# Kernel optimization log

Measured on AMD Instinct MI355X. Metric: run time of the kernel, lower is better.

The kernel has to match this reference:

```python
import jax, jax.numpy as jnp
import numpy as np
from jax import lax

B, CIN, S = 16, 1, 64          # batch, input channels, spatial
C = 16                          # c_out hidden channels
T = 50                          # ODE steps
DT = 0.5
NC = 7                          # n_classes
K = T // 2 + 1                  # rfft bins = 26
HID = 256


def conv2d_same(x, w, b):
    # x:(B,Ci,H,W) w:(Co,Ci,3,3) zero 'SAME' padding (torch padding=1)
    y = lax.conv_general_dilated(x, w, (1, 1), 'SAME',
                                 dimension_numbers=('NCHW', 'OIHW', 'NCHW'))
    return y + b[None, :, None, None]


def conv2d_circular(x, w):
    # circular padding=1, no bias (coRNNCell.Wy)
    xp = jnp.pad(x, ((0, 0), (0, 0), (1, 1), (1, 1)), mode='wrap')
    return lax.conv_general_dilated(xp, w, (1, 1), 'VALID',
                                    dimension_numbers=('NCHW', 'OIHW', 'NCHW'))


def setup_inputs() -> dict:
    key = jax.random.key(0)
    ks = iter(jax.random.split(key, 40))
    d = {}
    d['x'] = jax.random.normal(next(ks), (B, CIN, S, S), dtype=jnp.float32)

    def cw(ci, co):
        return jax.random.normal(next(ks), (co, ci, 3, 3), jnp.float32) * (1.0 / np.sqrt(ci * 9))

    # omega / alpha encoders: 3 convs each
    for p in ('om', 'al'):
        d[f'{p}_w1'], d[f'{p}_b1'] = cw(CIN, C), jnp.zeros((C,), jnp.float32)
        d[f'{p}_w2'], d[f'{p}_b2'] = cw(C, C), jnp.zeros((C,), jnp.float32)
        d[f'{p}_w3'], d[f'{p}_b3'] = cw(C, C), jnp.zeros((C,), jnp.float32)
    # hy encoder: 4 convs
    d['hy_w1'], d['hy_b1'] = cw(CIN, C), jnp.zeros((C,), jnp.float32)
    d['hy_w2'], d['hy_b2'] = cw(C, C), jnp.zeros((C,), jnp.float32)
    d['hy_w3'], d['hy_b3'] = cw(C, C), jnp.zeros((C,), jnp.float32)
    d['hy_w4'], d['hy_b4'] = cw(C, C), jnp.zeros((C,), jnp.float32)
    # cell conv: block-diagonal discrete Laplacian (per torch init)
    lap = np.array([[0., 1., 0.], [1., -4., 1.], [0., 1., 0.]], np.float32)
    wy = np.zeros((C, C, 3, 3), np.float32)
    wy[np.arange(C), np.arange(C)] = lap
    d['wy'] = jnp.asarray(wy)
    # readout MLP: 416 -> 256 -> 256 -> 256 -> 7
    dims = [K * C, HID, HID, HID, NC]
    for i in range(4):
        d[f'ro_w{i+1}'] = jax.random.normal(next(ks), (dims[i], dims[i + 1]), jnp.float32) * (1.0 / np.sqrt(dims[i]))
        d[f'ro_b{i+1}'] = jnp.zeros((dims[i + 1],), jnp.float32)
    return d


def _forward(x,
             om_w1, om_b1, om_w2, om_b2, om_w3, om_b3,
             al_w1, al_b1, al_w2, al_b2, al_w3, al_b3,
             hy_w1, hy_b1, hy_w2, hy_b2, hy_w3, hy_b3, hy_w4, hy_b4,
             wy,
             ro_w1, ro_b1, ro_w2, ro_b2, ro_w3, ro_b3, ro_w4, ro_b4):
    relu = jax.nn.relu
    # encoders
    om = relu(conv2d_same(relu(conv2d_same(relu(conv2d_same(x, om_w1, om_b1)), om_w2, om_b2)), om_w3, om_b3))
    al = relu(conv2d_same(relu(conv2d_same(relu(conv2d_same(x, al_w1, al_b1)), al_w2, al_b2)), al_w3, al_b3))
    h = relu(conv2d_same(x, hy_w1, hy_b1))
    h = relu(conv2d_same(h, hy_w2, hy_b2))
    h = relu(conv2d_same(h, hy_w3, hy_b3))
    hy0 = jnp.tanh(conv2d_same(h, hy_w4, hy_b4))

    omega = om.reshape(B, C, S * S)
    alpha = al.reshape(B, C, S * S)
    hy = hy0.reshape(B, C, S * S)
    hz = jnp.zeros_like(hy)

    def step(carry, _):
        hy, hz = carry
        sf = jnp.tanh(conv2d_circular(hy.reshape(B, C, S, S), wy)).reshape(B, C, S * S)
        new_hz = hz + DT * (sf - omega * hy - alpha * hz)
        new_hy = hy + DT * new_hz
        return (new_hy, new_hz), new_hy

    _, y_seq = lax.scan(step, (hy, hz), None, length=T)   # (T,B,C,HW)
    y_seq = jnp.transpose(y_seq, (1, 3, 2, 0)).reshape(B * S * S, C, T)  # (BHW,C,T)

    fft_mag = jnp.abs(jnp.fft.rfft(y_seq, axis=2))        # (BHW,C,K)
    f = fft_mag.reshape(B * S * S, C * K)                  # (BHW, C*K)

    f = relu(f @ ro_w1 + ro_b1)
    f = relu(f @ ro_w2 + ro_b2)
    f = relu(f @ ro_w3 + ro_b3)
    logits_flat = f @ ro_w4 + ro_b4                        # (BHW, NC)
    logits = logits_flat.reshape(B, S, S, NC).transpose(0, 3, 1, 2)
    return logits


def reference(x,
              om_w1, om_b1, om_w2, om_b2, om_w3, om_b3,
              al_w1, al_b1, al_w2, al_b2, al_w3, al_b3,
              hy_w1, hy_b1, hy_w2, hy_b2, hy_w3, hy_b3, hy_w4, hy_b4,
              wy,
              ro_w1, ro_b1, ro_w2, ro_b2, ro_w3, ro_b3, ro_w4, ro_b4):
    return _forward(x,
                    om_w1, om_b1, om_w2, om_b2, om_w3, om_b3,
                    al_w1, al_b1, al_w2, al_b2, al_w3, al_b3,
                    hy_w1, hy_b1, hy_w2, hy_b2, hy_w3, hy_b3, hy_w4, hy_b4,
                    wy,
                    ro_w1, ro_b1, ro_w2, ro_b2, ro_w3, ro_b3, ro_w4, ro_b4)
```

## Files before the change

### kernel.cpp

```cpp
#include <hip/hip_runtime.h>
#include <hip/hip_bf16.h>
#include <hip/hip_fp16.h>
#include <math.h>

#define B_   16
#define C_   16
#define S_   64
#define HW_  4096
#define T_   50
#define K_   26
#define F_   416
#define HID_ 256
#define NC_  7
#define DT_  0.5f
#define BCHW_ (B_*C_*HW_)
#define M_   (B_*HW_)

typedef short    bf16x8 __attribute__((ext_vector_type(8)));
typedef _Float16 f16x8  __attribute__((ext_vector_type(8)));
typedef float    f32x4  __attribute__((ext_vector_type(4)));

__device__ __forceinline__ void gld_lds16(const void* g, void* l){
    __builtin_amdgcn_global_load_lds(
        (const __attribute__((address_space(1))) void*)g,
        (__attribute__((address_space(3))) void*)l, 16, 0, 0);
}

__device__ __forceinline__ float fast_tanh(float x){
    float ax = fabsf(x);
    float e  = __expf(2.f*ax);
    float r  = 1.f - 2.f/(e + 1.f);
    return copysignf(r, x);
}

template<int CIN, int ACT>
__global__ __launch_bounds__(1024) void convf_kernel(
    const float* __restrict__ in0, const float* __restrict__ in1, const float* __restrict__ in2,
    const float* __restrict__ w0,  const float* __restrict__ w1,  const float* __restrict__ w2,
    const float* __restrict__ b0,  const float* __restrict__ b1,  const float* __restrict__ b2,
    float* __restrict__ o0, float* __restrict__ o1, float* __restrict__ o2)
{
    __shared__ float slab[CIN][18][66];
    const int slice = blockIdx.x;
    const int b     = blockIdx.y;
    const int ch    = blockIdx.z;
    const float* in = (ch == 0) ? in0 : (ch == 1) ? in1 : in2;
    const float* w  = (ch == 0) ? w0  : (ch == 1) ? w1  : w2;
    const float* bb = (ch == 0) ? b0  : (ch == 1) ? b1  : b2;
    float* out      = (ch == 0) ? o0  : (ch == 1) ? o1  : o2;

    const int tid = threadIdx.x;
    const int y0  = slice * 16;

    for (int idx = tid; idx < CIN*18*66; idx += 1024){
        int ci  = idx / (18*66);
        int rem = idx % (18*66);
        int rr  = rem / 66;
        int cc  = rem % 66;
        int gy = y0 - 1 + rr;
        int gx = cc - 1;
        float v = 0.f;
        if ((unsigned)gy < 64u && (unsigned)gx < 64u)
            v = in[(size_t)(b*CIN + ci)*HW_ + gy*64 + gx];
        slab[ci][rr][cc] = v;
    }
    __syncthreads();

    const int x  = tid & 63;
    const int ry = tid >> 6;

    float acc[16];
    #pragma unroll
    for (int co = 0; co < 16; co++) acc[co] = bb[co];

    for (int ci = 0; ci < CIN; ci++){
        float p[3][3];
        #pragma unroll
        for (int dy = 0; dy < 3; dy++)
            #pragma unroll
            for (int dx = 0; dx < 3; dx++)
                p[dy][dx] = slab[ci][ry + dy][x + dx];
        #pragma unroll
        for (int co = 0; co < 16; co++){
            const float* wp = w + (size_t)(co*CIN + ci)*9;
            float s = acc[co];
            #pragma unroll
            for (int dy = 0; dy < 3; dy++)
                #pragma unroll
                for (int dx = 0; dx < 3; dx++)
                    s = fmaf(wp[dy*3 + dx], p[dy][dx], s);
            acc[co] = s;
        }
    }
    #pragma unroll
    for (int co = 0; co < 16; co++){
        float v = acc[co];
        v = ACT ? fast_tanh(v) : fmaxf(v, 0.f);
        out[(size_t)(b*16 + co)*HW_ + (y0 + ry)*64 + x] = v;
    }
}

__global__ __launch_bounds__(1024) void ode_kernel(
    const float* __restrict__ omega, const float* __restrict__ alpha,
    const float* __restrict__ hy0,   const float* __restrict__ wy,
    __half* __restrict__ yseq)
{
    __shared__ float buf[2][64*65];
    const int blk = blockIdx.x;
    const int c   = blk & 15;
    const int tid = threadIdx.x;
    const int x   = tid & 63;
    const int sy  = (tid >> 6) << 2;
    const size_t off = (size_t)blk * HW_;

    float om[4], al[4], hz[4], hy[4];
    #pragma unroll
    for (int i = 0; i < 4; i++){
        size_t g = off + (size_t)(sy + i)*64 + x;
        om[i] = omega[g];
        al[i] = alpha[g];
        hz[i] = 0.f;
        hy[i] = hy0[g];
        buf[0][x*65 + sy + i] = hy[i];
    }
    float wv[9];
    const float* wp = wy + (size_t)(c*C_ + c)*9;
    #pragma unroll
    for (int j = 0; j < 9; j++) wv[j] = wp[j];
    __syncthreads();

    const int xl = ((x + 63) & 63) * 65;
    const int xr = ((x + 1)  & 63) * 65;
    const int xo = x * 65;
    const int ylo = (sy + 63) & 63;
    const int yhi = (sy + 4)  & 63;

    int cur = 0;
    for (int t = 0; t < T_; t++){
        const float* hp = buf[cur];
        float* hn = buf[cur ^ 1];
        float l[6], r[6];
        l[0] = hp[xl + ylo];  r[0] = hp[xr + ylo];
        #pragma unroll
        for (int i = 0; i < 4; i++){ l[i+1] = hp[xl + sy + i]; r[i+1] = hp[xr + sy + i]; }
        l[5] = hp[xl + yhi];  r[5] = hp[xr + yhi];
        float tN = hp[xo + ylo];
        float tS = hp[xo + yhi];

        __half* yout = yseq + (size_t)t*BCHW_ + off;
        float ny[4];
        #pragma unroll
        for (int i = 0; i < 4; i++){
            float up = (i == 0) ? tN : hy[i-1];
            float dn = (i == 3) ? tS : hy[i+1];
            float s = wv[0]*l[i]   + wv[1]*up    + wv[2]*r[i]
                    + wv[3]*l[i+1] + wv[4]*hy[i] + wv[5]*r[i+1]
                    + wv[6]*l[i+2] + wv[7]*dn    + wv[8]*r[i+2];
            float sf = fast_tanh(s);
            float nz = hz[i] + DT_*(sf - om[i]*hy[i] - al[i]*hz[i]);
            float v  = hy[i] + DT_*nz;
            hz[i] = nz;
            ny[i] = v;
        }
        #pragma unroll
        for (int i = 0; i < 4; i++){
            hy[i] = ny[i];
            hn[xo + sy + i] = ny[i];
            yout[(sy + i)*64 + x] = __float2half(ny[i]);
        }
        __syncthreads();
        cur ^= 1;
    }
}

__global__ __launch_bounds__(256) void dft_mfma_kernel(
    const __half* __restrict__ yseq, __hip_bfloat16* __restrict__ f)
{
    __shared__ char Ys[8*256*16];
    __shared__ char Gs[8*64*16];
    const int tid = threadIdx.x;
    const int blk = blockIdx.x;
    const int bc  = blk >> 4;
    const int p0  = (blk & 15) << 8;
    const int b   = bc >> 4, c = bc & 15;

    for (int idx = tid; idx < 64*64; idx += 256){
        int r = idx >> 6, t = idx & 63;
        float v = 0.f;
        if (r < 52 && t < 50){
            int k  = r >> 1;
            int ph = (k * t) % 50;
            float ang = (float)ph * (6.2831853071795864f / 50.f);
            v = (r & 1) ? sinf(ang) : cosf(ang);
        }
        *(_Float16*)(Gs + ((t >> 3)*64 + r)*16 + (t & 7)*2) = (_Float16)v;
    }

    {
        const __half* src = yseq + (size_t)bc*HW_ + p0 + tid;
        #pragma unroll
        for (int t2 = 0; t2 < 25; t2++){
            unsigned int a = *(const unsigned short*)&src[(size_t)(2*t2)*BCHW_];
            unsigned int d = *(const unsigned short*)&src[(size_t)(2*t2+1)*BCHW_];
            int t8 = t2 >> 2, j = t2 & 3;
            *(unsigned int*)(Ys + (t8*256 + tid)*16 + j*4) = a | (d << 16);
        }
        #pragma unroll
        for (int t2 = 25; t2 < 32; t2++){
            int t8 = t2 >> 2, j = t2 & 3;
            *(unsigned int*)(Ys + (t8*256 + tid)*16 + j*4) = 0u;
        }
    }
    __syncthreads();

    const int lane = tid & 63;
    const int w    = tid >> 6;
    const int n    = lane & 15;
    const int quad = lane >> 4;
    const int mrow = 16*w + n;

    f16x8 a0 = *(const f16x8*)(Gs + ((quad    )*64 + mrow)*16);
    f16x8 a1 = *(const f16x8*)(Gs + ((quad + 4)*64 + mrow)*16);

    const int kb0   = 8*w + 2*quad;
    const bool valid = (kb0 < K_);

    for (int nt = 0; nt < 16; nt++){
        f16x8 b0 = *(const f16x8*)(Ys + ((quad    )*256 + nt*16 + n)*16);
        f16x8 b1 = *(const f16x8*)(Ys + ((quad + 4)*256 + nt*16 + n)*16);
        f32x4 acc = (f32x4){0.f, 0.f, 0.f, 0.f};
        acc = __builtin_amdgcn_mfma_f32_16x16x32_f16(a0, b0, acc, 0, 0, 0);
        acc = __builtin_amdgcn_mfma_f32_16x16x32_f16(a1, b1, acc, 0, 0, 0);
        if (valid){
            float m0 = sqrtf(fmaf(acc[0], acc[0], acc[1]*acc[1]));
            float m1 = sqrtf(fmaf(acc[2], acc[2], acc[3]*acc[3]));
            __hip_bfloat16 h0 = __float2bfloat16(m0);
            __hip_bfloat16 h1 = __float2bfloat16(m1);
            unsigned int u = ((unsigned int)*(unsigned short*)&h1 << 16)
                           |  (unsigned int)*(unsigned short*)&h0;
            const int row = b*HW_ + p0 + nt*16 + n;
            *(unsigned int*)((char*)(f + (size_t)row*F_ + c*K_) + kb0*2) = u;
        }
    }
}

__global__ __launch_bounds__(256) void prep_wt_kernel(
    const float* __restrict__ w, __hip_bfloat16* __restrict__ wt, int Kd, int N)
{
    const int n = blockIdx.x;
    for (int k = threadIdx.x; k < Kd; k += 256)
        wt[(size_t)n*Kd + k] = __float2bfloat16(w[(size_t)k*N + n]);
}

__global__ __launch_bounds__(256) void gemm_mfma_kernel(
    const __hip_bfloat16* __restrict__ A, const __hip_bfloat16* __restrict__ Wt,
    const float* __restrict__ bias, __hip_bfloat16* __restrict__ C,
    int M, int N, int Kd)
{
    __shared__ short As[128*32];
    __shared__ short Bs[128*32];
    const int tid  = threadIdx.x;
    const int lane = tid & 63;
    const int wave = tid >> 6;
    const int wm = (wave & 1) * 64;
    const int wn = (wave >> 1) * 64;
    const int m0 = blockIdx.x * 128;
    const int n0 = blockIdx.y * 128;

    f32x4 acc[4][4];
    #pragma unroll
    for (int i = 0; i < 4; i++)
        #pragma unroll
        for (int j = 0; j < 4; j++)
            acc[i][j] = (f32x4){0.f, 0.f, 0.f, 0.f};

    const int rloc = tid >> 2;
    const int kc   = (tid & 3) * 8;
    const char* Ag = (const char*)(A  + (size_t)(m0 + rloc)*Kd + kc);
    const char* Bg = (const char*)(Wt + (size_t)(n0 + rloc)*Kd + kc);
    const size_t rstride = (size_t)64 * Kd * 2;
    char* AsB = (char*)As + tid*16;
    char* BsB = (char*)Bs + tid*16;

    const int fa = (wm + (lane & 15)) * 32 + (lane >> 4) * 8;
    const int fb = (wn + (lane & 15)) * 32 + (lane >> 4) * 8;

    for (int k0 = 0; k0 < Kd; k0 += 32){
        const char* ag = Ag + (size_t)k0 * 2;
        const char* bg = Bg + (size_t)k0 * 2;
        gld_lds16(ag,           AsB);
        gld_lds16(ag + rstride, AsB + 4096);
        gld_lds16(bg,           BsB);
        gld_lds16(bg + rstride, BsB + 4096);
        __syncthreads();

        bf16x8 af[4], bfv[4];
        #pragma unroll
        for (int i = 0; i < 4; i++){
            af[i]  = *(const bf16x8*)&As[fa + i*16*32];
            bfv[i] = *(const bf16x8*)&Bs[fb + i*16*32];
        }
        #pragma unroll
        for (int i = 0; i < 4; i++)
            #pragma unroll
            for (int j = 0; j < 4; j++)
                acc[i][j] = __builtin_amdgcn_mfma_f32_16x16x32_bf16(
                                af[i], bfv[j], acc[i][j], 0, 0, 0);
        __syncthreads();
    }

    const int colb = n0 + wn + (lane & 15);
    const int rowb = m0 + wm + ((lane >> 4) << 2);
    #pragma unroll
    for (int j = 0; j < 4; j++){
        const int col = colb + j*16;
        const float bv = bias[col];
        #pragma unroll
        for (int i = 0; i < 4; i++){
            const int row0 = rowb + i*16;
            #pragma unroll
            for (int r = 0; r < 4; r++){
                float v = acc[i][j][r] + bv;
                v = fmaxf(v, 0.f);
                C[(size_t)(row0 + r)*N + col] = __float2bfloat16(v);
            }
        }
    }
}

__global__ __launch_bounds__(256) void final_kernel(
    const __hip_bfloat16* __restrict__ h, const float* __restrict__ w,
    const float* __restrict__ bias, float* __restrict__ out)
{
    __shared__ float wsm[HID_*NC_];
    __shared__ float bs[NC_];
    const int tid = threadIdx.x;
    for (int i = tid; i < HID_*NC_; i += 256) wsm[i] = w[i];
    if (tid < NC_) bs[tid] = bias[tid];
    __syncthreads();

    const int row = blockIdx.x*256 + tid;
    const uint4* hp = (const uint4*)(h + (size_t)row*HID_);
    float acc[NC_];
    #pragma unroll
    for (int j = 0; j < NC_; j++) acc[j] = bs[j];

    for (int k8 = 0; k8 < HID_/8; k8++){
        uint4 u = hp[k8];
        float v[8];
        v[0] = __uint_as_float(u.x << 16); v[1] = __uint_as_float(u.x & 0xffff0000u);
        v[2] = __uint_as_float(u.y << 16); v[3] = __uint_as_float(u.y & 0xffff0000u);
        v[4] = __uint_as_float(u.z << 16); v[5] = __uint_as_float(u.z & 0xffff0000u);
        v[6] = __uint_as_float(u.w << 16); v[7] = __uint_as_float(u.w & 0xffff0000u);
        const int k = k8*8;
        #pragma unroll
        for (int e = 0; e < 8; e++){
            #pragma unroll
            for (int j = 0; j < NC_; j++)
                acc[j] = fmaf(v[e], wsm[(k+e)*NC_ + j], acc[j]);
        }
    }
    const int b = row >> 12, hw = row & 4095;
    #pragma unroll
    for (int j = 0; j < NC_; j++)
        out[(size_t)(b*NC_ + j)*HW_ + hw] = acc[j];
}

extern "C" void kernel_launch(void* const* d_in, const int* in_sizes, int n_in,
                              void* d_out, int out_size, void* d_ws, size_t ws_size,
                              hipStream_t stream)
{
    const float* x     = (const float*)d_in[0];
    const float* om_w1 = (const float*)d_in[1];  const float* om_b1 = (const float*)d_in[2];
    const float* om_w2 = (const float*)d_in[3];  const float* om_b2 = (const float*)d_in[4];
    const float* om_w3 = (const float*)d_in[5];  const float* om_b3 = (const float*)d_in[6];
    const float* al_w1 = (const float*)d_in[7];  const float* al_b1 = (const float*)d_in[8];
    const float* al_w2 = (const float*)d_in[9];  const float* al_b2 = (const float*)d_in[10];
    const float* al_w3 = (const float*)d_in[11]; const float* al_b3 = (const float*)d_in[12];
    const float* hy_w1 = (const float*)d_in[13]; const float* hy_b1 = (const float*)d_in[14];
    const float* hy_w2 = (const float*)d_in[15]; const float* hy_b2 = (const float*)d_in[16];
    const float* hy_w3 = (const float*)d_in[17]; const float* hy_b3 = (const float*)d_in[18];
    const float* hy_w4 = (const float*)d_in[19]; const float* hy_b4 = (const float*)d_in[20];
    const float* wy    = (const float*)d_in[21];
    const float* ro_w1 = (const float*)d_in[22]; const float* ro_b1 = (const float*)d_in[23];
    const float* ro_w2 = (const float*)d_in[24]; const float* ro_b2 = (const float*)d_in[25];
    const float* ro_w3 = (const float*)d_in[26]; const float* ro_b3 = (const float*)d_in[27];
    const float* ro_w4 = (const float*)d_in[28]; const float* ro_b4 = (const float*)d_in[29];
    float* out = (float*)d_out;

    char* wsb = (char*)d_ws;
    const size_t YSEQ_BYTES = (size_t)T_ * BCHW_ * 2;
    __half* yseq = (__half*)wsb;
    __hip_bfloat16* fbuf = (__hip_bfloat16*)(wsb + YSEQ_BYTES);

    const size_t MB4 = (size_t)BCHW_ * 4;
    float* om_t1 = (float*)(wsb + YSEQ_BYTES + 0*MB4);
    float* al_t1 = (float*)(wsb + YSEQ_BYTES + 1*MB4);
    float* hy_t1 = (float*)(wsb + YSEQ_BYTES + 2*MB4);
    float* om_t2 = (float*)(wsb + YSEQ_BYTES + 3*MB4);
    float* al_t2 = (float*)(wsb + YSEQ_BYTES + 4*MB4);
    float* hy_t2 = (float*)(wsb + YSEQ_BYTES + 5*MB4);
    float* omega = (float*)(wsb + YSEQ_BYTES + 6*MB4);
    float* alpha = (float*)(wsb + YSEQ_BYTES + 7*MB4);
    float* hy_t3 = (float*)(wsb + YSEQ_BYTES + 8*MB4);
    float* hy0   = (float*)(wsb + YSEQ_BYTES + 9*MB4);

    const size_t HB = (size_t)M_ * HID_ * 2;
    __hip_bfloat16* h1 = (__hip_bfloat16*)(wsb + 0);
    __hip_bfloat16* h2 = (__hip_bfloat16*)(wsb + HB);
    __hip_bfloat16* h3 = (__hip_bfloat16*)(wsb + 2*HB);
    __hip_bfloat16* wt1 = (__hip_bfloat16*)(wsb + 3*HB);
    __hip_bfloat16* wt2 = (__hip_bfloat16*)(wsb + 3*HB + 212992);
    __hip_bfloat16* wt3 = (__hip_bfloat16*)(wsb + 3*HB + 344064);

    convf_kernel<1,0><<<dim3(4,B_,3), 1024, 0, stream>>>(
        x, x, x, om_w1, al_w1, hy_w1, om_b1, al_b1, hy_b1, om_t1, al_t1, hy_t1);
    convf_kernel<16,0><<<dim3(4,B_,3), 1024, 0, stream>>>(
        om_t1, al_t1, hy_t1, om_w2, al_w2, hy_w2, om_b2, al_b2, hy_b2, om_t2, al_t2, hy_t2);
    convf_kernel<16,0><<<dim3(4,B_,3), 1024, 0, stream>>>(
        om_t2, al_t2, hy_t2, om_w3, al_w3, hy_w3, om_b3, al_b3, hy_b3, omega, alpha, hy_t3);
    convf_kernel<16,1><<<dim3(4,B_,1), 1024, 0, stream>>>(
        hy_t3, hy_t3, hy_t3, hy_w4, hy_w4, hy_w4, hy_b4, hy_b4, hy_b4, hy0, hy0, hy0);
    ode_kernel<<<256, 1024, 0, stream>>>(omega, alpha, hy0, wy, yseq);
    dft_mfma_kernel<<<4096, 256, 0, stream>>>(yseq, fbuf);
    prep_wt_kernel<<<256, 256, 0, stream>>>(ro_w1, wt1, F_,   HID_);
    prep_wt_kernel<<<256, 256, 0, stream>>>(ro_w2, wt2, HID_, HID_);
    prep_wt_kernel<<<256, 256, 0, stream>>>(ro_w3, wt3, HID_, HID_);
    gemm_mfma_kernel<<<dim3(512,2), 256, 0, stream>>>(fbuf, wt1, ro_b1, h1, M_, HID_, F_);
    gemm_mfma_kernel<<<dim3(512,2), 256, 0, stream>>>(h1,   wt2, ro_b2, h2, M_, HID_, HID_);
    gemm_mfma_kernel<<<dim3(512,2), 256, 0, stream>>>(h2,   wt3, ro_b3, h3, M_, HID_, HID_);
    final_kernel<<<256, 256, 0, stream>>>(h3, ro_w4, ro_b4, out);
}
```

Before: 437.5 us.

## Fuse readout MLP into one LDS-resident kernel and skip zero stencil corner taps

The three bf16 GEMM layers and the final 256->7 projection are replaced by a single kernel. Each 512-thread block keeps a 256-row tile of hidden activations in LDS across all layers. This removes the global-memory round trips for the h1/h2/h3 intermediates and three kernel launches. The trade-off is roughly 155 KB of LDS per block and only 256 blocks, so each CU holds a single low-occupancy block and there is less latency hiding. Separately, the ODE stencil checks at runtime whether the four corner weights are zero and, if so, skips those neighbour loads and multiply-adds; for non-zero corner weights it falls back to the full nine-tap stencil.

```diff
diff --git a/kernel.cpp b/kernel.cpp
--- a/kernel.cpp
+++ b/kernel.cpp
@@ -33,6 +33,14 @@
     return copysignf(r, x);
 }
 
+__device__ __forceinline__ float b2f(short s){
+    return __uint_as_float(((unsigned int)(unsigned short)s) << 16);
+}
+__device__ __forceinline__ short f2b(float f){
+    __hip_bfloat16 h = __float2bfloat16(f);
+    return *(short*)&h;
+}
+
 template<int CIN, int ACT>
 __global__ __launch_bounds__(1024) void convf_kernel(
     const float* __restrict__ in0, const float* __restrict__ in1, const float* __restrict__ in2,
@@ -127,6 +135,7 @@
     const float* wp = wy + (size_t)(c*C_ + c)*9;
     #pragma unroll
     for (int j = 0; j < 9; j++) wv[j] = wp[j];
+    const bool five = (wv[0]==0.f) & (wv[2]==0.f) & (wv[6]==0.f) & (wv[8]==0.f);
     __syncthreads();
 
     const int xl = ((x + 63) & 63) * 65;
@@ -140,10 +149,12 @@
         const float* hp = buf[cur];
         float* hn = buf[cur ^ 1];
         float l[6], r[6];
-        l[0] = hp[xl + ylo];  r[0] = hp[xr + ylo];
         #pragma unroll
         for (int i = 0; i < 4; i++){ l[i+1] = hp[xl + sy + i]; r[i+1] = hp[xr + sy + i]; }
-        l[5] = hp[xl + yhi];  r[5] = hp[xr + yhi];
+        if (!five){
+            l[0] = hp[xl + ylo];  r[0] = hp[xr + ylo];
+            l[5] = hp[xl + yhi];  r[5] = hp[xr + yhi];
+        }
         float tN = hp[xo + ylo];
         float tS = hp[xo + yhi];
 
@@ -153,9 +164,9 @@
         for (int i = 0; i < 4; i++){
             float up = (i == 0) ? tN : hy[i-1];
             float dn = (i == 3) ? tS : hy[i+1];
-            float s = wv[0]*l[i]   + wv[1]*up    + wv[2]*r[i]
-                    + wv[3]*l[i+1] + wv[4]*hy[i] + wv[5]*r[i+1]
-                    + wv[6]*l[i+2] + wv[7]*dn    + wv[8]*r[i+2];
+            float s = wv[1]*up + wv[3]*l[i+1] + wv[4]*hy[i] + wv[5]*r[i+1] + wv[7]*dn;
+            if (!five)
+                s += wv[0]*l[i] + wv[2]*r[i] + wv[6]*l[i+2] + wv[8]*r[i+2];
             float sf = fast_tanh(s);
             float nz = hz[i] + DT_*(sf - om[i]*hy[i] - al[i]*hz[i]);
             float v  = hy[i] + DT_*nz;
@@ -234,10 +245,8 @@
         if (valid){
             float m0 = sqrtf(fmaf(acc[0], acc[0], acc[1]*acc[1]));
             float m1 = sqrtf(fmaf(acc[2], acc[2], acc[3]*acc[3]));
-            __hip_bfloat16 h0 = __float2bfloat16(m0);
-            __hip_bfloat16 h1 = __float2bfloat16(m1);
-            unsigned int u = ((unsigned int)*(unsigned short*)&h1 << 16)
-                           |  (unsigned int)*(unsigned short*)&h0;
+            unsigned int u = ((unsigned int)(unsigned short)f2b(m1) << 16)
+                           |  (unsigned int)(unsigned short)f2b(m0);
             const int row = b*HW_ + p0 + nt*16 + n;
             *(unsigned int*)((char*)(f + (size_t)row*F_ + c*K_) + kb0*2) = u;
         }
@@ -252,118 +261,160 @@
         wt[(size_t)n*Kd + k] = __float2bfloat16(w[(size_t)k*N + n]);
 }
 
-__global__ __launch_bounds__(256) void gemm_mfma_kernel(
-    const __hip_bfloat16* __restrict__ A, const __hip_bfloat16* __restrict__ Wt,
-    const float* __restrict__ bias, __hip_bfloat16* __restrict__ C,
-    int M, int N, int Kd)
-{
-    __shared__ short As[128*32];
-    __shared__ short Bs[128*32];
+__global__ __launch_bounds__(512, 2) void mlp_fused_kernel(
+    const __hip_bfloat16* __restrict__ A,
+    const __hip_bfloat16* __restrict__ Wt1,
+    const __hip_bfloat16* __restrict__ Wt2,
+    const __hip_bfloat16* __restrict__ Wt3,
+    const float* __restrict__ b1, const float* __restrict__ b2,
+    const float* __restrict__ b3,
+    const float* __restrict__ w4, const float* __restrict__ b4,
+    float* __restrict__ out)
+{
+    __shared__ short hbuf[256*258];
+    __shared__ short Bs[1024*8];
+    __shared__ float w4s[HID_*NC_];
+
     const int tid  = threadIdx.x;
     const int lane = tid & 63;
     const int wave = tid >> 6;
-    const int wm = (wave & 1) * 64;
-    const int wn = (wave >> 1) * 64;
-    const int m0 = blockIdx.x * 128;
-    const int n0 = blockIdx.y * 128;
-
-    f32x4 acc[4][4];
+    const int wm   = (wave & 3) * 64;
+    const int wn   = (wave >> 2) * 128;
+    const int n16  = lane & 15;
+    const int quad = lane >> 4;
+    const int m0   = blockIdx.x * 256;
+
+    for (int i = tid; i < HID_*NC_; i += 512) w4s[i] = w4[i];
+
+    const int id0 = tid, id1 = tid + 512;
+    const int kc0 = id0 >> 8, nn0 = id0 & 255;
+    const int kc1 = id1 >> 8, nn1 = id1 & 255;
+
+    f32x4 acc[4][8];
     #pragma unroll
     for (int i = 0; i < 4; i++)
         #pragma unroll
-        for (int j = 0; j < 4; j++)
-            acc[i][j] = (f32x4){0.f, 0.f, 0.f, 0.f};
-
-    const int rloc = tid >> 2;
-    const int kc   = (tid & 3) * 8;
-    const char* Ag = (const char*)(A  + (size_t)(m0 + rloc)*Kd + kc);
-    const char* Bg = (const char*)(Wt + (size_t)(n0 + rloc)*Kd + kc);
-    const size_t rstride = (size_t)64 * Kd * 2;
-    char* AsB = (char*)As + tid*16;
-    char* BsB = (char*)Bs + tid*16;
-
-    const int fa = (wm + (lane & 15)) * 32 + (lane >> 4) * 8;
-    const int fb = (wn + (lane & 15)) * 32 + (lane >> 4) * 8;
-
-    for (int k0 = 0; k0 < Kd; k0 += 32){
-        const char* ag = Ag + (size_t)k0 * 2;
-        const char* bg = Bg + (size_t)k0 * 2;
-        gld_lds16(ag,           AsB);
-        gld_lds16(ag + rstride, AsB + 4096);
-        gld_lds16(bg,           BsB);
-        gld_lds16(bg + rstride, BsB + 4096);
+        for (int j = 0; j < 8; j++)
+            acc[i][j] = (f32x4){0.f,0.f,0.f,0.f};
+
+    const __hip_bfloat16* arow[4];
+    #pragma unroll
+    for (int i = 0; i < 4; i++)
+        arow[i] = A + (size_t)(m0 + wm + i*16 + n16)*F_ + quad*8;
+
+    bf16x8 afn[4];
+    #pragma unroll
+    for (int i = 0; i < 4; i++) afn[i] = *(const bf16x8*)(arow[i]);
+
+    for (int k0 = 0; k0 < F_; k0 += 32){
+        gld_lds16(Wt1 + (size_t)nn0*F_ + k0 + kc0*8, (char*)Bs + id0*16);
+        gld_lds16(Wt1 + (size_t)nn1*F_ + k0 + kc1*8, (char*)Bs + id1*16);
         __syncthreads();
-
-        bf16x8 af[4], bfv[4];
+        bf16x8 af[4];
+        #pragma unroll
+        for (int i = 0; i < 4; i++) af[i] = afn[i];
+        if (k0 + 32 < F_){
+            #pragma unroll
+            for (int i = 0; i < 4; i++) afn[i] = *(const bf16x8*)(arow[i] + k0 + 32);
+        }
+        bf16x8 bf[8];
+        #pragma unroll
+        for (int j = 0; j < 8; j++)
+            bf[j] = *(const bf16x8*)&Bs[(quad*256 + wn + j*16 + n16)*8];
+        #pragma unroll
+        for (int i = 0; i < 4; i++)
+            #pragma unroll
+            for (int j = 0; j < 8; j++)
+                acc[i][j] = __builtin_amdgcn_mfma_f32_16x16x32_bf16(
+                                af[i], bf[j], acc[i][j], 0, 0, 0);
+        __syncthreads();
+    }
+    #pragma unroll
+    for (int j = 0; j < 8; j++){
+        const int col = wn + j*16 + n16;
+        const float bv = b1[col];
         #pragma unroll
         for (int i = 0; i < 4; i++){
-            af[i]  = *(const bf16x8*)&As[fa + i*16*32];
-            bfv[i] = *(const bf16x8*)&Bs[fb + i*16*32];
-        }
+            const int r0 = wm + i*16 + quad*4;
+            #pragma unroll
+            for (int r = 0; r < 4; r++)
+                hbuf[(r0 + r)*258 + col] = f2b(fmaxf(acc[i][j][r] + bv, 0.f));
+        }
+    }
+    __syncthreads();
+
+    const __hip_bfloat16* Wts[2] = {Wt2, Wt3};
+    const float* bls[2] = {b2, b3};
+    for (int L = 0; L < 2; L++){
+        const __hip_bfloat16* Wt = Wts[L];
         #pragma unroll
         for (int i = 0; i < 4; i++)
             #pragma unroll
-            for (int j = 0; j < 4; j++)
-                acc[i][j] = __builtin_amdgcn_mfma_f32_16x16x32_bf16(
-                                af[i], bfv[j], acc[i][j], 0, 0, 0);
+            for (int j = 0; j < 8; j++)
+                acc[i][j] = (f32x4){0.f,0.f,0.f,0.f};
+
+        for (int k0 = 0; k0 < HID_; k0 += 32){
+            gld_lds16(Wt + (size_t)nn0*HID_ + k0 + kc0*8, (char*)Bs + id0*16);
+            gld_lds16(Wt + (size_t)nn1*HID_ + k0 + kc1*8, (char*)Bs + id1*16);
+            bf16x8 af[4];
+            #pragma unroll
+            for (int i = 0; i < 4; i++)
+                af[i] = *(const bf16x8*)&hbuf[(wm + i*16 + n16)*258 + k0 + quad*8];
+            __syncthreads();
+            bf16x8 bf[8];
+            #pragma unroll
+            for (int j = 0; j < 8; j++)
+                bf[j] = *(const bf16x8*)&Bs[(quad*256 + wn + j*16 + n16)*8];
+            #pragma unroll
+            for (int i = 0; i < 4; i++)
+                #pragma unroll
+                for (int j = 0; j < 8; j++)
+                    acc[i][j] = __builtin_amdgcn_mfma_f32_16x16x32_bf16(
+                                    af[i], bf[j], acc[i][j], 0, 0, 0);
+            __syncthreads();
+        }
+        const float* bl = bls[L];
+        #pragma unroll
+        for (int j = 0; j < 8; j++){
+            const int col = wn + j*16 + n16;
+            const float bv = bl[col];
+            #pragma unroll
+            for (int i = 0; i < 4; i++){
+                const int r0 = wm + i*16 + quad*4;
+                #pragma unroll
+                for (int r = 0; r < 4; r++)
+                    hbuf[(r0 + r)*258 + col] = f2b(fmaxf(acc[i][j][r] + bv, 0.f));
+            }
+        }
         __syncthreads();
     }
 
-    const int colb = n0 + wn + (lane & 15);
-    const int rowb = m0 + wm + ((lane >> 4) << 2);
-    #pragma unroll
-    for (int j = 0; j < 4; j++){
-        const int col = colb + j*16;
-        const float bv = bias[col];
-        #pragma unroll
-        for (int i = 0; i < 4; i++){
-            const int row0 = rowb + i*16;
-            #pragma unroll
-            for (int r = 0; r < 4; r++){
-                float v = acc[i][j][r] + bv;
-                v = fmaxf(v, 0.f);
-                C[(size_t)(row0 + r)*N + col] = __float2bfloat16(v);
-            }
-        }
-    }
-}
-
-__global__ __launch_bounds__(256) void final_kernel(
-    const __hip_bfloat16* __restrict__ h, const float* __restrict__ w,
-    const float* __restrict__ bias, float* __restrict__ out)
-{
-    __shared__ float wsm[HID_*NC_];
-    __shared__ float bs[NC_];
-    const int tid = threadIdx.x;
-    for (int i = tid; i < HID_*NC_; i += 256) wsm[i] = w[i];
-    if (tid < NC_) bs[tid] = bias[tid];
-    __syncthreads();
-
-    const int row = blockIdx.x*256 + tid;
-    const uint4* hp = (const uint4*)(h + (size_t)row*HID_);
-    float acc[NC_];
-    #pragma unroll
-    for (int j = 0; j < NC_; j++) acc[j] = bs[j];
+    const int row = tid >> 1;
+    const int sel = tid & 1;
+    const int j0  = sel ? 4 : 0;
+    const int nj  = sel ? 3 : 4;
+
+    float facc[4];
+    #pragma unroll
+    for (int t = 0; t < 4; t++) facc[t] = (t < nj) ? b4[j0 + t] : 0.f;
 
     for (int k8 = 0; k8 < HID_/8; k8++){
-        uint4 u = hp[k8];
-        float v[8];
-        v[0] = __uint_as_float(u.x << 16); v[1] = __uint_as_float(u.x & 0xffff0000u);
-        v[2] = __uint_as_float(u.y << 16); v[3] = __uint_as_float(u.y & 0xffff0000u);
-        v[4] = __uint_as_float(u.z << 16); v[5] = __uint_as_float(u.z & 0xffff0000u);
-        v[6] = __uint_as_float(u.w << 16); v[7] = __uint_as_float(u.w & 0xffff0000u);
-        const int k = k8*8;
+        bf16x8 hv = *(const bf16x8*)&hbuf[row*258 + k8*8];
         #pragma unroll
         for (int e = 0; e < 8; e++){
-            #pragma unroll
-            for (int j = 0; j < NC_; j++)
-                acc[j] = fmaf(v[e], wsm[(k+e)*NC_ + j], acc[j]);
-        }
-    }
-    const int b = row >> 12, hw = row & 4095;
-    #pragma unroll
-    for (int j = 0; j < NC_; j++)
-        out[(size_t)(b*NC_ + j)*HW_ + hw] = acc[j];
+            float vv = b2f(hv[e]);
+            const float* wr = &w4s[(k8*8 + e)*NC_ + j0];
+            #pragma unroll
+            for (int t = 0; t < 4; t++)
+                if (t < nj) facc[t] = fmaf(vv, wr[t], facc[t]);
+        }
+    }
+    const int grow = m0 + row;
+    const int bidx = grow >> 12, hw = grow & 4095;
+    #pragma unroll
+    for (int t = 0; t < 4; t++)
+        if (t < nj)
+            out[(size_t)(bidx*NC_ + j0 + t)*HW_ + hw] = facc[t];
 }
 
 extern "C" void kernel_launch(void* const* d_in, const int* in_sizes, int n_in,
@@ -405,13 +456,9 @@
     float* hy_t3 = (float*)(wsb + YSEQ_BYTES + 8*MB4);
     float* hy0   = (float*)(wsb + YSEQ_BYTES + 9*MB4);
 
-    const size_t HB = (size_t)M_ * HID_ * 2;
-    __hip_bfloat16* h1 = (__hip_bfloat16*)(wsb + 0);
-    __hip_bfloat16* h2 = (__hip_bfloat16*)(wsb + HB);
-    __hip_bfloat16* h3 = (__hip_bfloat16*)(wsb + 2*HB);
-    __hip_bfloat16* wt1 = (__hip_bfloat16*)(wsb + 3*HB);
-    __hip_bfloat16* wt2 = (__hip_bfloat16*)(wsb + 3*HB + 212992);
-    __hip_bfloat16* wt3 = (__hip_bfloat16*)(wsb + 3*HB + 344064);
+    __hip_bfloat16* wt1 = (__hip_bfloat16*)(wsb + 0);
+    __hip_bfloat16* wt2 = (__hip_bfloat16*)(wsb + 212992);
+    __hip_bfloat16* wt3 = (__hip_bfloat16*)(wsb + 344064);
 
     convf_kernel<1,0><<<dim3(4,B_,3), 1024, 0, stream>>>(
         x, x, x, om_w1, al_w1, hy_w1, om_b1, al_b1, hy_b1, om_t1, al_t1, hy_t1);
@@ -426,8 +473,6 @@
     prep_wt_kernel<<<256, 256, 0, stream>>>(ro_w1, wt1, F_,   HID_);
     prep_wt_kernel<<<256, 256, 0, stream>>>(ro_w2, wt2, HID_, HID_);
     prep_wt_kernel<<<256, 256, 0, stream>>>(ro_w3, wt3, HID_, HID_);
-    gemm_mfma_kernel<<<dim3(512,2), 256, 0, stream>>>(fbuf, wt1, ro_b1, h1, M_, HID_, F_);
-    gemm_mfma_kernel<<<dim3(512,2), 256, 0, stream>>>(h1,   wt2, ro_b2, h2, M_, HID_, HID_);
-    gemm_mfma_kernel<<<dim3(512,2), 256, 0, stream>>>(h2,   wt3, ro_b3, h3, M_, HID_, HID_);
-    final_kernel<<<256, 256, 0, stream>>>(h3, ro_w4, ro_b4, out);
-}
+    mlp_fused_kernel<<<256, 512, 0, stream>>>(
+        fbuf, wt1, wt2, wt3, ro_b1, ro_b2, ro_b3, ro_w4, ro_b4, out);
+}
```

Result: faster. 413.9 us (-5.4%).
